# Kernel optimization log

Hardware: AMD Instinct MI355X
Metric: run time of the kernel (lower is better)

## Reference

```python
import jax, jax.numpy as jnp
import numpy as np

D_MODEL = 1024
NHEAD = 16
HEAD_DIM = D_MODEL // NHEAD
D_FF = 4096
BIAS_HID = 8
EPS = 1e-5


def _pair_bias(m, w1, b1, w2, b2):
    # m: [B,S,S] -> bias [B,S,S,nhead] via per-scalar MLP 1->hid->nhead
    h = jax.nn.relu(m[..., None] * w1 + b1)          # [B,S,S,hid]
    return jnp.einsum('bxyh,hn->bxyn', h, w2) + b2   # [B,S,S,nhead]


def _layernorm(x, g, b):
    mu = jnp.mean(x, axis=-1, keepdims=True)
    var = jnp.mean(jnp.square(x - mu), axis=-1, keepdims=True)
    return (x - mu) * jax.lax.rsqrt(var + EPS) * g + b


def setup_inputs() -> dict:
    key = jax.random.key(0)
    ks = jax.random.split(key, 20)
    B, S = 4, 1024
    sc = 1.0 / np.sqrt(D_MODEL)
    inp = {
        'src': jax.random.normal(ks[0], (B, S, D_MODEL), jnp.float32),
        't_deltas': jax.random.uniform(ks[1], (B, S, S), jnp.float32),
        'dists': jax.random.uniform(ks[2], (B, S, S), jnp.float32),
        'Wq': jax.random.normal(ks[3], (D_MODEL, D_MODEL), jnp.float32) * sc,
        'bq': jnp.zeros((D_MODEL,), jnp.float32),
        'Wk': jax.random.normal(ks[4], (D_MODEL, D_MODEL), jnp.float32) * sc,
        'bk': jnp.zeros((D_MODEL,), jnp.float32),
        'Wv': jax.random.normal(ks[5], (D_MODEL, D_MODEL), jnp.float32) * sc,
        'bv': jnp.zeros((D_MODEL,), jnp.float32),
        'tb_w1': jax.random.normal(ks[6], (BIAS_HID,), jnp.float32),
        'tb_b1': jnp.zeros((BIAS_HID,), jnp.float32),
        'tb_w2': jax.random.normal(ks[7], (BIAS_HID, NHEAD), jnp.float32) * 0.3,
        'tb_b2': jnp.zeros((NHEAD,), jnp.float32),
        'db_w1': jax.random.normal(ks[8], (BIAS_HID,), jnp.float32),
        'db_b1': jnp.zeros((BIAS_HID,), jnp.float32),
        'db_w2': jax.random.normal(ks[9], (BIAS_HID, NHEAD), jnp.float32) * 0.3,
        'db_b2': jnp.zeros((NHEAD,), jnp.float32),
        'W1': jax.random.normal(ks[10], (D_MODEL, D_FF), jnp.float32) * sc,
        'b1': jnp.zeros((D_FF,), jnp.float32),
        'W2': jax.random.normal(ks[11], (D_FF, D_MODEL), jnp.float32) / np.sqrt(D_FF),
        'b2': jnp.zeros((D_MODEL,), jnp.float32),
        'g1': jnp.ones((D_MODEL,), jnp.float32),
        'beta1': jnp.zeros((D_MODEL,), jnp.float32),
        'g2': jnp.ones((D_MODEL,), jnp.float32),
        'beta2': jnp.zeros((D_MODEL,), jnp.float32),
    }
    return inp


def reference(src, t_deltas, dists, Wq, bq, Wk, bk, Wv, bv,
              tb_w1, tb_b1, tb_w2, tb_b2, db_w1, db_b1, db_w2, db_b2,
              W1, b1, W2, b2, g1, beta1, g2, beta2):
    B, S, _ = src.shape
    # QKV projections -> [B, H, S, hd]
    q = (src @ Wq + bq).reshape(B, S, NHEAD, HEAD_DIM).transpose(0, 2, 1, 3)
    k = (src @ Wk + bk).reshape(B, S, NHEAD, HEAD_DIM).transpose(0, 2, 1, 3)
    v = (src @ Wv + bv).reshape(B, S, NHEAD, HEAD_DIM).transpose(0, 2, 1, 3)
    # scores scaled by sqrt(d_model) (as in the original, not head_dim)
    scores = jnp.einsum('bhqd,bhkd->bhqk', q, k) / jnp.sqrt(jnp.float32(D_MODEL))
    bias = (_pair_bias(t_deltas, tb_w1, tb_b1, tb_w2, tb_b2)
            + _pair_bias(dists, db_w1, db_b1, db_w2, db_b2))  # [B,S,S,H]
    scores = scores + bias.transpose(0, 3, 1, 2)
    attn = jax.nn.softmax(scores, axis=-1)
    out = jnp.einsum('bhqk,bhkd->bhqd', attn, v)
    out = out.transpose(0, 2, 1, 3).reshape(B, S, D_MODEL)
    x = _layernorm(src + out, g1, beta1)
    ffn = jax.nn.relu(x @ W1 + b1) @ W2 + b2
    return _layernorm(x + ffn, g2, beta2)
```

## Files before the change

kernel.cpp:

```cpp
#include <hip/hip_runtime.h>

typedef __bf16 bf16x8 __attribute__((ext_vector_type(8)));
typedef float f32x4 __attribute__((ext_vector_type(4)));
typedef unsigned short u16;

__device__ __forceinline__ u16 f2bf(float f) {
  union { float f; unsigned u; } x; x.f = f;
  unsigned r = x.u + 0x7fffu + ((x.u >> 16) & 1u);
  return (u16)(r >> 16);
}
__device__ __forceinline__ float bf2f(u16 u) {
  union { unsigned u; float f; } x; x.u = ((unsigned)u) << 16;
  return x.f;
}
__device__ __forceinline__ void gl_lds16(const void* g, void* l) {
  __builtin_amdgcn_global_load_lds(
      (const __attribute__((address_space(1))) void*)g,
      (__attribute__((address_space(3))) void*)l, 16, 0, 0);
}

__global__ __launch_bounds__(256) void cvt_kernel(const float* __restrict__ in,
                                                  u16* __restrict__ out, int n4) {
  int i = blockIdx.x * 256 + threadIdx.x;
  if (i >= n4) return;
  float4 v = ((const float4*)in)[i];
  unsigned lo = (unsigned)f2bf(v.x) | ((unsigned)f2bf(v.y) << 16);
  unsigned hi = (unsigned)f2bf(v.z) | ((unsigned)f2bf(v.w) << 16);
  uint2 u; u.x = lo; u.y = hi;
  *(uint2*)&out[(size_t)i * 4] = u;
}

__global__ __launch_bounds__(256) void tconv_kernel(const float* __restrict__ in,
                                                    u16* __restrict__ out, int R, int C) {
  __shared__ float tile[32][33];
  int c0 = blockIdx.x * 32, r0 = blockIdx.y * 32;
  int tx = threadIdx.x & 31, ty = threadIdx.x >> 5;
#pragma unroll
  for (int i = 0; i < 4; i++)
    tile[ty + i * 8][tx] = in[(size_t)(r0 + ty + i * 8) * C + c0 + tx];
  __syncthreads();
#pragma unroll
  for (int i = 0; i < 4; i++)
    out[(size_t)(c0 + ty + i * 8) * R + r0 + tx] = f2bf(tile[tx][ty + i * 8]);
}

__global__ __launch_bounds__(256) void tconv3_kernel(const float* __restrict__ w0,
                                                     const float* __restrict__ w1,
                                                     const float* __restrict__ w2,
                                                     u16* __restrict__ out) {
  __shared__ float tile[32][33];
  int mat = blockIdx.y >> 5;
  const float* in = mat == 0 ? w0 : (mat == 1 ? w1 : w2);
  u16* o = out + (size_t)mat * 1024 * 1024;
  int c0 = blockIdx.x * 32, r0 = (blockIdx.y & 31) * 32;
  int tx = threadIdx.x & 31, ty = threadIdx.x >> 5;
#pragma unroll
  for (int i = 0; i < 4; i++)
    tile[ty + i * 8][tx] = in[(size_t)(r0 + ty + i * 8) * 1024 + c0 + tx];
  __syncthreads();
#pragma unroll
  for (int i = 0; i < 4; i++)
    o[(size_t)(c0 + ty + i * 8) * 1024 + r0 + tx] = f2bf(tile[tx][ty + i * 8]);
}

template <int EPI>
__global__ __launch_bounds__(256) void gemm128_kernel(const u16* __restrict__ A,
                                                      const u16* __restrict__ Bt,
                                                      const float* __restrict__ bias,
                                                      const float* __restrict__ biasK,
                                                      const float* __restrict__ biasV,
                                                      void* __restrict__ out,
                                                      int M, int N, int K,
                                                      float qscale, int kslice) {
  __shared__ u16 lds[3][2][4096];
  int tid = threadIdx.x, w = tid >> 6, lane = tid & 63;
  int l16 = lane & 15, lhi = lane >> 4;
  int wr = w >> 1, wc = w & 1;
  int GX = gridDim.x;
  int nwg = GX * gridDim.y;
  int nlin = blockIdx.y * GX + blockIdx.x;
  int cpx = nwg >> 3;
  int sw = (nlin & 7) * cpx + (nlin >> 3);
  int m0 = (sw / GX) * 128, n0 = (sw % GX) * 128;
  int z = blockIdx.z;
  const u16* Ag = A + (size_t)m0 * K + z * kslice;
  const u16* Bg = Bt + (size_t)n0 * K + z * kslice;
  f32x4 acc[4][4] = {};
  int np = kslice >> 5;

  int srow = tid >> 2;
  int sxor = ((tid & 3) ^ ((tid >> 3) & 3)) * 8;
  int rga = (lhi ^ ((l16 >> 1) & 3)) * 8;

  auto stageP = [&](int slot, int p) {
    const u16* As = Ag + (size_t)p * 32 + sxor;
    const u16* Bs = Bg + (size_t)p * 32 + sxor;
#pragma unroll
    for (int ld = 0; ld < 2; ld++)
      gl_lds16(As + (size_t)(ld * 64 + srow) * K, &lds[slot][0][ld * 2048 + w * 512]);
#pragma unroll
    for (int ld = 0; ld < 2; ld++)
      gl_lds16(Bs + (size_t)(ld * 64 + srow) * K, &lds[slot][1][ld * 2048 + w * 512]);
  };
  auto rdAB = [&](int slot, bf16x8 (&af)[4], bf16x8 (&bfr)[4]) {
#pragma unroll
    for (int m = 0; m < 4; m++)
      af[m] = *(const bf16x8*)&lds[slot][0][(wr * 64 + m * 16 + l16) * 32 + rga];
#pragma unroll
    for (int nn = 0; nn < 4; nn++)
      bfr[nn] = *(const bf16x8*)&lds[slot][1][(wc * 64 + nn * 16 + l16) * 32 + rga];
  };
  auto mma16 = [&](bf16x8 (&af)[4], bf16x8 (&bfr)[4]) {
    __builtin_amdgcn_s_setprio(1);
#pragma unroll
    for (int m = 0; m < 4; m++)
#pragma unroll
      for (int nn = 0; nn < 4; nn++)
        acc[m][nn] =
            __builtin_amdgcn_mfma_f32_16x16x32_bf16(af[m], bfr[nn], acc[m][nn], 0, 0, 0);
    __builtin_amdgcn_s_setprio(0);
  };

  stageP(0, 0);
  stageP(1, 1);

  int slot = 0;
  for (int p = 0; p < np; ++p) {
    bf16x8 af[4], bfr[4];
    if (p + 1 < np) asm volatile("s_waitcnt vmcnt(4)" ::: "memory");
    else            asm volatile("s_waitcnt vmcnt(0)" ::: "memory");
    __builtin_amdgcn_s_barrier();
    rdAB(slot, af, bfr);
    if (p + 2 < np) {
      int s2 = slot + 2; if (s2 >= 3) s2 -= 3;
      stageP(s2, p + 2);
    }
    asm volatile("s_waitcnt lgkmcnt(0)" ::: "memory");
    __builtin_amdgcn_sched_barrier(0);
    mma16(af, bfr);
    if (++slot == 3) slot = 0;
  }

#pragma unroll
  for (int m = 0; m < 4; m++) {
    int gr = m0 + wr * 64 + m * 16 + lhi * 4;
#pragma unroll
    for (int nn = 0; nn < 4; nn++) {
      int gc = n0 + wc * 64 + nn * 16 + l16;
      float bv;
      if (EPI == 2) {
        int seg = gc >> 10, c = gc & 1023;
        bv = seg == 0 ? bias[c] : (seg == 1 ? biasK[c] : biasV[c]);
        int h = c >> 6, d = c & 63;
        float sc = (seg == 0) ? qscale : 1.f;
#pragma unroll
        for (int r = 0; r < 4; r++) {
          int row = gr + r;
          int b = row >> 10, s = row & 1023;
          size_t idx = ((((size_t)seg * 4 + b) * 16 + h) * 1024 + s) * 64 + d;
          ((u16*)out)[idx] = f2bf((acc[m][nn][r] + bv) * sc);
        }
      } else if (EPI == 1) {
        bv = bias[gc];
#pragma unroll
        for (int r = 0; r < 4; r++)
          ((u16*)out)[(size_t)(gr + r) * N + gc] = f2bf(fmaxf(acc[m][nn][r] + bv, 0.f));
      } else if (EPI == 3) {
        bv = (z == 0 && bias) ? bias[gc] : 0.f;
#pragma unroll
        for (int r = 0; r < 4; r++)
          ((u16*)out)[(size_t)z * M * N + (size_t)(gr + r) * N + gc] = f2bf(acc[m][nn][r] + bv);
      } else {
        bv = (z == 0 && bias) ? bias[gc] : 0.f;
#pragma unroll
        for (int r = 0; r < 4; r++)
          ((float*)out)[(size_t)z * M * N + (size_t)(gr + r) * N + gc] = acc[m][nn][r] + bv;
      }
    }
  }
}

__global__ __launch_bounds__(256) void vtrans_kernel(const u16* __restrict__ v,
                                                     u16* __restrict__ vt) {
  __shared__ u16 t[64][72];
  int bh = blockIdx.y, s0 = blockIdx.x * 64;
  int tid = threadIdx.x;
  int r = tid >> 2, c = (tid & 3) * 16;
  const u16* src = v + ((size_t)bh * 1024 + s0 + r) * 64 + c;
  *(int4*)&t[r][c] = *(const int4*)src;
  *(int4*)&t[r][c + 8] = *(const int4*)(src + 8);
  __syncthreads();
  int d = tid >> 2, sc = (tid & 3) * 16;
  u16 tmp[16];
#pragma unroll
  for (int j = 0; j < 16; j++) tmp[j] = t[sc + j][d];
  u16* dst = vt + ((size_t)bh * 64 + d) * 1024 + s0 + sc;
  *(int4*)dst = *(int4*)&tmp[0];
  *(int4*)(dst + 8) = *(int4*)&tmp[8];
}

#define LOG2E 1.44269504088896f
__global__ __launch_bounds__(256) void bias_kernel(
    const float* __restrict__ td, const float* __restrict__ dd,
    const float* __restrict__ tw1, const float* __restrict__ tb1,
    const float* __restrict__ tw2, const float* __restrict__ tb2,
    const float* __restrict__ dw1, const float* __restrict__ db1,
    const float* __restrict__ dw2, const float* __restrict__ db2,
    u16* __restrict__ biasout, int b0) {
  __shared__ float stw2[128], sdw2[128], sb2[16];
  __shared__ float stw1[8], stb1[8], sdw1[8], sdb1[8];
  int tid = threadIdx.x, x = blockIdx.x, bz = blockIdx.y;
  int b = b0 + bz;
  if (tid < 128) { stw2[tid] = tw2[tid]; sdw2[tid] = dw2[tid]; }
  if (tid < 16) sb2[tid] = tb2[tid] + db2[tid];
  if (tid < 8) { stw1[tid] = tw1[tid]; stb1[tid] = tb1[tid]; sdw1[tid] = dw1[tid]; sdb1[tid] = db1[tid]; }
  __syncthreads();
  float4 tv = ((const float4*)(td + ((size_t)b * 1024 + x) * 1024))[tid];
  float4 dv = ((const float4*)(dd + ((size_t)b * 1024 + x) * 1024))[tid];
  float tj[4] = {tv.x, tv.y, tv.z, tv.w};
  float dj[4] = {dv.x, dv.y, dv.z, dv.w};
  float ht[4][8], hd[4][8];
#pragma unroll
  for (int j = 0; j < 4; j++)
#pragma unroll
    for (int i = 0; i < 8; i++) {
      ht[j][i] = fmaxf(tj[j] * stw1[i] + stb1[i], 0.f);
      hd[j][i] = fmaxf(dj[j] * sdw1[i] + sdb1[i], 0.f);
    }
  u16* outb = biasout + (size_t)bz * 16 * 1024 * 1024 + (size_t)x * 1024 + tid * 4;
#pragma unroll
  for (int h = 0; h < 16; h++) {
    float a[4];
#pragma unroll
    for (int j = 0; j < 4; j++) {
      float s = sb2[h];
#pragma unroll
      for (int i = 0; i < 8; i++)
        s += ht[j][i] * stw2[i * 16 + h] + hd[j][i] * sdw2[i * 16 + h];
      a[j] = s * LOG2E;
    }
    unsigned lo = (unsigned)f2bf(a[0]) | ((unsigned)f2bf(a[1]) << 16);
    unsigned hi = (unsigned)f2bf(a[2]) | ((unsigned)f2bf(a[3]) << 16);
    uint2 u; u.x = lo; u.y = hi;
    *(uint2*)&outb[(size_t)h * 1024 * 1024] = u;
  }
}

#define LDA 72
#define SMC 12.0f
__global__ __launch_bounds__(256) void attn_kernel(
    const u16* __restrict__ qg, const u16* __restrict__ kg, const u16* __restrict__ vtg,
    const u16* __restrict__ bias, float* __restrict__ attn_out, int b0) {
  __shared__ u16 Ks[64 * LDA];
  __shared__ u16 Vt[64 * LDA];
  __shared__ u16 Ps[64 * LDA];
  int tid = threadIdx.x;
  int w = tid >> 6, l = tid & 63, l16 = l & 15, lhi = l >> 4;
  int qt = blockIdx.x, h = blockIdx.y, bz = blockIdx.z;
  int b = b0 + bz;
  size_t bh = ((size_t)(b * 16 + h)) * 1024 * 64;
  const u16* biasb = bias + (size_t)bz * 16 * 1024 * 1024 + (size_t)h * 1024 * 1024;
  int qrow = qt * 64 + w * 16 + l16;
  bf16x8 qa[2];
  qa[0] = *(const bf16x8*)&qg[bh + (size_t)qrow * 64 + lhi * 8];
  qa[1] = *(const bf16x8*)&qg[bh + (size_t)qrow * 64 + 32 + lhi * 8];

  float l_part[4] = {0.f, 0.f, 0.f, 0.f};
  f32x4 o[4] = {};

  int kr0 = (tid * 2) >> 3, kc0 = ((tid * 2) & 7) * 8;
  int kr1 = (tid * 2 + 1) >> 3, kc1 = ((tid * 2 + 1) & 7) * 8;
  const u16* kbase = kg + bh;
  const u16* vbase = vtg + bh;

  int4 kA, kB, vA, vB;
  u16 bpre[16];
  auto issueKV = [&](int kt) {
    kA = *(const int4*)&kbase[(size_t)(kt * 64 + kr0) * 64 + kc0];
    kB = *(const int4*)&kbase[(size_t)(kt * 64 + kr1) * 64 + kc1];
    vA = *(const int4*)&vbase[(size_t)kr0 * 1024 + kt * 64 + kc0];
    vB = *(const int4*)&vbase[(size_t)kr1 * 1024 + kt * 64 + kc1];
  };
  auto issueBias = [&](int kt) {
#pragma unroll
    for (int ni = 0; ni < 4; ni++)
#pragma unroll
      for (int r = 0; r < 4; r++)
        bpre[ni * 4 + r] =
            biasb[(size_t)(qt * 64 + w * 16 + lhi * 4 + r) * 1024 + kt * 64 + ni * 16 + l16];
  };
  issueKV(0);
  issueBias(0);

  for (int kt = 0; kt < 16; kt++) {
    __syncthreads();
    *(int4*)&Ks[kr0 * LDA + kc0] = kA;
    *(int4*)&Ks[kr1 * LDA + kc1] = kB;
    *(int4*)&Vt[kr0 * LDA + kc0] = vA;
    *(int4*)&Vt[kr1 * LDA + kc1] = vB;
    __syncthreads();
    u16 bcur[16];
#pragma unroll
    for (int i = 0; i < 16; i++) bcur[i] = bpre[i];
    if (kt + 1 < 16) { issueKV(kt + 1); issueBias(kt + 1); }
    __builtin_amdgcn_sched_barrier(0);

    f32x4 s[4] = {};
    __builtin_amdgcn_s_setprio(1);
#pragma unroll
    for (int ni = 0; ni < 4; ni++)
#pragma unroll
      for (int ks = 0; ks < 2; ks++) {
        bf16x8 kb = *(const bf16x8*)&Ks[(ni * 16 + l16) * LDA + ks * 32 + lhi * 8];
        s[ni] = __builtin_amdgcn_mfma_f32_16x16x32_bf16(qa[ks], kb, s[ni], 0, 0, 0);
      }
    __builtin_amdgcn_s_setprio(0);
#pragma unroll
    for (int ni = 0; ni < 4; ni++)
#pragma unroll
      for (int r = 0; r < 4; r++) {
        float p = exp2f(s[ni][r] + bf2f(bcur[ni * 4 + r]) - SMC);
        l_part[r] += p;
        Ps[(w * 16 + lhi * 4 + r) * LDA + ni * 16 + l16] = f2bf(p);
      }
    __builtin_amdgcn_s_setprio(1);
#pragma unroll
    for (int ks = 0; ks < 2; ks++) {
      bf16x8 pa = *(const bf16x8*)&Ps[(w * 16 + l16) * LDA + ks * 32 + lhi * 8];
#pragma unroll
      for (int di = 0; di < 4; di++) {
        bf16x8 vb = *(const bf16x8*)&Vt[(di * 16 + l16) * LDA + ks * 32 + lhi * 8];
        o[di] = __builtin_amdgcn_mfma_f32_16x16x32_bf16(pa, vb, o[di], 0, 0, 0);
      }
    }
    __builtin_amdgcn_s_setprio(0);
  }
#pragma unroll
  for (int r = 0; r < 4; r++) {
    float lr = l_part[r];
    lr += __shfl_xor(lr, 1, 16);
    lr += __shfl_xor(lr, 2, 16);
    lr += __shfl_xor(lr, 4, 16);
    lr += __shfl_xor(lr, 8, 16);
    float inv = 1.f / lr;
    int row = b * 1024 + qt * 64 + w * 16 + lhi * 4 + r;
#pragma unroll
    for (int di = 0; di < 4; di++)
      attn_out[(size_t)row * 1024 + h * 64 + di * 16 + l16] = o[di][r] * inv;
  }
}

__global__ __launch_bounds__(256) void ln_kernel(const float* __restrict__ a,
                                                 const float* __restrict__ r1,
                                                 const float* __restrict__ g,
                                                 const float* __restrict__ beta,
                                                 float* __restrict__ outf,
                                                 u16* __restrict__ outbf) {
  int row = blockIdx.x, tid = threadIdx.x;
  __shared__ float red[8];
  float4 va = ((const float4*)(a + (size_t)row * 1024))[tid];
  float4 vr = ((const float4*)(r1 + (size_t)row * 1024))[tid];
  float v[4] = {va.x + vr.x, va.y + vr.y, va.z + vr.z, va.w + vr.w};
  float s = v[0] + v[1] + v[2] + v[3];
#pragma unroll
  for (int off = 32; off >= 1; off >>= 1) s += __shfl_xor(s, off, 64);
  if ((tid & 63) == 0) red[tid >> 6] = s;
  __syncthreads();
  float mean = (red[0] + red[1] + red[2] + red[3]) * (1.f / 1024.f);
  float q = 0.f;
#pragma unroll
  for (int j = 0; j < 4; j++) { float d = v[j] - mean; q += d * d; }
#pragma unroll
  for (int off = 32; off >= 1; off >>= 1) q += __shfl_xor(q, off, 64);
  if ((tid & 63) == 0) red[4 + (tid >> 6)] = q;
  __syncthreads();
  float var = (red[4] + red[5] + red[6] + red[7]) * (1.f / 1024.f);
  float rstd = rsqrtf(var + 1e-5f);
  float4 gv = ((const float4*)g)[tid];
  float4 bv = ((const float4*)beta)[tid];
  float o0 = (v[0] - mean) * rstd * gv.x + bv.x;
  float o1 = (v[1] - mean) * rstd * gv.y + bv.y;
  float o2 = (v[2] - mean) * rstd * gv.z + bv.z;
  float o3 = (v[3] - mean) * rstd * gv.w + bv.w;
  float4 ov; ov.x = o0; ov.y = o1; ov.z = o2; ov.w = o3;
  ((float4*)(outf + (size_t)row * 1024))[tid] = ov;
  unsigned lo = (unsigned)f2bf(o0) | ((unsigned)f2bf(o1) << 16);
  unsigned hi = (unsigned)f2bf(o2) | ((unsigned)f2bf(o3) << 16);
  uint2 u; u.x = lo; u.y = hi;
  *(uint2*)&outbf[(size_t)row * 1024 + tid * 4] = u;
}

__global__ __launch_bounds__(256) void ln2_kernel(const float* __restrict__ x,
                                                  const u16* __restrict__ ff, int zs,
                                                  const float* __restrict__ g,
                                                  const float* __restrict__ beta,
                                                  float* __restrict__ out) {
  int row = blockIdx.x, tid = threadIdx.x;
  __shared__ float red[8];
  float4 xv = ((const float4*)(x + (size_t)row * 1024))[tid];
  float v[4] = {xv.x, xv.y, xv.z, xv.w};
  for (int z = 0; z < zs; z++) {
    uint2 u = *(const uint2*)&ff[(size_t)z * 4096 * 1024 + (size_t)row * 1024 + tid * 4];
    v[0] += bf2f(u.x & 0xffff); v[1] += bf2f(u.x >> 16);
    v[2] += bf2f(u.y & 0xffff); v[3] += bf2f(u.y >> 16);
  }
  float s = v[0] + v[1] + v[2] + v[3];
#pragma unroll
  for (int off = 32; off >= 1; off >>= 1) s += __shfl_xor(s, off, 64);
  if ((tid & 63) == 0) red[tid >> 6] = s;
  __syncthreads();
  float mean = (red[0] + red[1] + red[2] + red[3]) * (1.f / 1024.f);
  float q = 0.f;
#pragma unroll
  for (int j = 0; j < 4; j++) { float d = v[j] - mean; q += d * d; }
#pragma unroll
  for (int off = 32; off >= 1; off >>= 1) q += __shfl_xor(q, off, 64);
  if ((tid & 63) == 0) red[4 + (tid >> 6)] = q;
  __syncthreads();
  float var = (red[4] + red[5] + red[6] + red[7]) * (1.f / 1024.f);
  float rstd = rsqrtf(var + 1e-5f);
  float4 gv = ((const float4*)g)[tid];
  float4 bv = ((const float4*)beta)[tid];
  float4 ov;
  ov.x = (v[0] - mean) * rstd * gv.x + bv.x;
  ov.y = (v[1] - mean) * rstd * gv.y + bv.y;
  ov.z = (v[2] - mean) * rstd * gv.z + bv.z;
  ov.w = (v[3] - mean) * rstd * gv.w + bv.w;
  ((float4*)(out + (size_t)row * 1024))[tid] = ov;
}

extern "C" void kernel_launch(void* const* d_in, const int* in_sizes, int n_in,
                              void* d_out, int out_size, void* d_ws, size_t ws_size,
                              hipStream_t stream) {
  const float* src      = (const float*)d_in[0];
  const float* t_deltas = (const float*)d_in[1];
  const float* dists    = (const float*)d_in[2];
  const float* Wq = (const float*)d_in[3];
  const float* bq = (const float*)d_in[4];
  const float* Wk = (const float*)d_in[5];
  const float* bk = (const float*)d_in[6];
  const float* Wv = (const float*)d_in[7];
  const float* bv = (const float*)d_in[8];
  const float* tb_w1 = (const float*)d_in[9];
  const float* tb_b1 = (const float*)d_in[10];
  const float* tb_w2 = (const float*)d_in[11];
  const float* tb_b2 = (const float*)d_in[12];
  const float* db_w1 = (const float*)d_in[13];
  const float* db_b1 = (const float*)d_in[14];
  const float* db_w2 = (const float*)d_in[15];
  const float* db_b2 = (const float*)d_in[16];
  const float* W1 = (const float*)d_in[17];
  const float* b1 = (const float*)d_in[18];
  const float* W2 = (const float*)d_in[19];
  const float* b2 = (const float*)d_in[20];
  const float* g1 = (const float*)d_in[21];
  const float* beta1 = (const float*)d_in[22];
  const float* g2 = (const float*)d_in[23];
  const float* beta2 = (const float*)d_in[24];
  float* out = (float*)d_out;

  const size_t MB = 1024u * 1024;
  bool huge = ws_size >= 210 * MB;
  bool big  = ws_size >= 150 * MB;
  int PB = huge ? 4 : (big ? 2 : 1);
  const int ZS = 2;

  char* ws = (char*)d_ws;
  size_t off = 0;
  auto alloc = [&](size_t n) { void* p = ws + off; off += (n + 255) & ~(size_t)255; return p; };
  u16* src_bf  = (u16*)alloc(4096u * 1024 * 2);
  u16* wqkv_bt = (u16*)alloc(3072u * 1024 * 2);
  u16* w1_bt   = (u16*)alloc(4096u * 1024 * 2);
  u16* w2_bt   = (u16*)alloc(1024u * 4096 * 2);
  u16* qkv     = (u16*)alloc(3u * 4 * 16 * 1024 * 64 * 2);
  u16* vt      = (u16*)alloc(4u * 16 * 64 * 1024 * 2);
  u16* slab    = (u16*)alloc((size_t)PB * 16 * 1024 * 1024 * 2);
  float* attn_out = (float*)alloc(4096u * 1024 * 4);
  (void)in_sizes; (void)n_in; (void)out_size;

  u16* q_bf = qkv;
  u16* k_bf = qkv + 4u * 16 * 1024 * 64;
  u16* v_bf = qkv + 8u * 16 * 1024 * 64;
  float* x_f32 = (float*)qkv;
  u16*   x_bf  = (u16*)((char*)qkv + 16 * MB);
  u16*   h_bf  = (u16*)vt;
  u16*   ffnb  = (u16*)attn_out;

  cvt_kernel<<<4096, 256, 0, stream>>>(src, src_bf, 4096 * 1024 / 4);
  tconv3_kernel<<<dim3(32, 96), 256, 0, stream>>>(Wq, Wk, Wv, wqkv_bt);
  tconv_kernel<<<dim3(128, 32), 256, 0, stream>>>(W1, w1_bt, 1024, 4096);
  tconv_kernel<<<dim3(32, 128), 256, 0, stream>>>(W2, w2_bt, 4096, 1024);

  gemm128_kernel<2><<<dim3(24, 32, 1), 256, 0, stream>>>(src_bf, wqkv_bt, bq, bk, bv, qkv,
                                                         4096, 3072, 1024,
                                                         1.44269504088896f / 32.f, 1024);
  vtrans_kernel<<<dim3(16, 64), 256, 0, stream>>>(v_bf, vt);

  for (int p = 0; p < 4 / PB; p++) {
    bias_kernel<<<dim3(1024, PB), 256, 0, stream>>>(t_deltas, dists, tb_w1, tb_b1, tb_w2, tb_b2,
                                                    db_w1, db_b1, db_w2, db_b2, slab, p * PB);
    attn_kernel<<<dim3(16, 16, PB), 256, 0, stream>>>(q_bf, k_bf, vt, slab, attn_out, p * PB);
  }

  ln_kernel<<<4096, 256, 0, stream>>>(src, attn_out, g1, beta1, x_f32, x_bf);
  gemm128_kernel<1><<<dim3(32, 32, 1), 256, 0, stream>>>(x_bf, w1_bt, b1, nullptr, nullptr, h_bf,
                                                         4096, 4096, 1024, 1.f, 1024);
  gemm128_kernel<3><<<dim3(8, 32, ZS), 256, 0, stream>>>(h_bf, w2_bt, b2, nullptr, nullptr, ffnb,
                                                         4096, 1024, 4096, 1.f, 4096 / ZS);
  ln2_kernel<<<4096, 256, 0, stream>>>(x_f32, ffnb, ZS, g2, beta2, out);
}
```

Baseline: 281.2 us.

## Store pair bias in MFMA fragment order for vectorized attention loads

The bias kernel now writes the bf16 bias slab in the per-thread fragment order used by the attention kernel's MFMA accumulator layout. Each attention thread can then fetch its 16 bias values with two 16-byte loads instead of 16 scattered 2-byte loads. The trade-off is that the bias kernel now reads t_deltas and dists with strided scalar loads instead of coalesced float4 row loads, and the grid is reshaped to 16x16 tiles. The bias index inside the softmax loop is permuted to match the new packing.

After: 612.1 us. 2.18x slower.

```diff
diff --git a/kernel.cpp b/kernel.cpp
--- a/kernel.cpp
+++ b/kernel.cpp
@@ -209,40 +209,49 @@
     u16* __restrict__ biasout, int b0) {
   __shared__ float stw2[128], sdw2[128], sb2[16];
   __shared__ float stw1[8], stb1[8], sdw1[8], sdb1[8];
-  int tid = threadIdx.x, x = blockIdx.x, bz = blockIdx.y;
+  int tid = threadIdx.x;
+  int kt = blockIdx.x, qt = blockIdx.y, bz = blockIdx.z;
   int b = b0 + bz;
   if (tid < 128) { stw2[tid] = tw2[tid]; sdw2[tid] = dw2[tid]; }
   if (tid < 16) sb2[tid] = tb2[tid] + db2[tid];
   if (tid < 8) { stw1[tid] = tw1[tid]; stb1[tid] = tb1[tid]; sdw1[tid] = dw1[tid]; sdb1[tid] = db1[tid]; }
   __syncthreads();
-  float4 tv = ((const float4*)(td + ((size_t)b * 1024 + x) * 1024))[tid];
-  float4 dv = ((const float4*)(dd + ((size_t)b * 1024 + x) * 1024))[tid];
-  float tj[4] = {tv.x, tv.y, tv.z, tv.w};
-  float dj[4] = {dv.x, dv.y, dv.z, dv.w};
-  float ht[4][8], hd[4][8];
-#pragma unroll
-  for (int j = 0; j < 4; j++)
-#pragma unroll
-    for (int i = 0; i < 8; i++) {
-      ht[j][i] = fmaxf(tj[j] * stw1[i] + stb1[i], 0.f);
-      hd[j][i] = fmaxf(dj[j] * sdw1[i] + sdb1[i], 0.f);
+  int w = tid >> 6, l = tid & 63, lhi = l >> 4, l16 = l & 15;
+  u16* outb = biasout + ((((size_t)bz * 16 * 16 + qt) * 16 + kt) * 256 + tid) * 16;
+  const size_t hstride = (size_t)16 * 16 * 256 * 16;
+
+#pragma unroll
+  for (int r = 0; r < 4; r++) {
+    int x = qt * 64 + w * 16 + lhi * 4 + r;
+    const float* trow = td + ((size_t)b * 1024 + x) * 1024 + kt * 64 + l16;
+    const float* drow = dd + ((size_t)b * 1024 + x) * 1024 + kt * 64 + l16;
+    float tj[4], dj[4];
+#pragma unroll
+    for (int ni = 0; ni < 4; ni++) { tj[ni] = trow[ni * 16]; dj[ni] = drow[ni * 16]; }
+    float ht[4][8], hd[4][8];
+#pragma unroll
+    for (int ni = 0; ni < 4; ni++)
+#pragma unroll
+      for (int i = 0; i < 8; i++) {
+        ht[ni][i] = fmaxf(tj[ni] * stw1[i] + stb1[i], 0.f);
+        hd[ni][i] = fmaxf(dj[ni] * sdw1[i] + sdb1[i], 0.f);
+      }
+#pragma unroll
+    for (int h = 0; h < 16; h++) {
+      float a[4];
+#pragma unroll
+      for (int ni = 0; ni < 4; ni++) {
+        float s = sb2[h];
+#pragma unroll
+        for (int i = 0; i < 8; i++)
+          s += ht[ni][i] * stw2[i * 16 + h] + hd[ni][i] * sdw2[i * 16 + h];
+        a[ni] = s * LOG2E;
+      }
+      uint2 u;
+      u.x = (unsigned)f2bf(a[0]) | ((unsigned)f2bf(a[1]) << 16);
+      u.y = (unsigned)f2bf(a[2]) | ((unsigned)f2bf(a[3]) << 16);
+      *(uint2*)&outb[hstride * h + r * 4] = u;
     }
-  u16* outb = biasout + (size_t)bz * 16 * 1024 * 1024 + (size_t)x * 1024 + tid * 4;
-#pragma unroll
-  for (int h = 0; h < 16; h++) {
-    float a[4];
-#pragma unroll
-    for (int j = 0; j < 4; j++) {
-      float s = sb2[h];
-#pragma unroll
-      for (int i = 0; i < 8; i++)
-        s += ht[j][i] * stw2[i * 16 + h] + hd[j][i] * sdw2[i * 16 + h];
-      a[j] = s * LOG2E;
-    }
-    unsigned lo = (unsigned)f2bf(a[0]) | ((unsigned)f2bf(a[1]) << 16);
-    unsigned hi = (unsigned)f2bf(a[2]) | ((unsigned)f2bf(a[3]) << 16);
-    uint2 u; u.x = lo; u.y = hi;
-    *(uint2*)&outb[(size_t)h * 1024 * 1024] = u;
   }
 }
 
@@ -259,7 +268,7 @@
   int qt = blockIdx.x, h = blockIdx.y, bz = blockIdx.z;
   int b = b0 + bz;
   size_t bh = ((size_t)(b * 16 + h)) * 1024 * 64;
-  const u16* biasb = bias + (size_t)bz * 16 * 1024 * 1024 + (size_t)h * 1024 * 1024;
+  const u16* bfragbase = bias + ((((size_t)(bz * 16 + h) * 16 + qt) * 16) * 256 + tid) * 16;
   int qrow = qt * 64 + w * 16 + l16;
   bf16x8 qa[2];
   qa[0] = *(const bf16x8*)&qg[bh + (size_t)qrow * 64 + lhi * 8];
@@ -274,7 +283,7 @@
   const u16* vbase = vtg + bh;
 
   int4 kA, kB, vA, vB;
-  u16 bpre[16];
+  int4 bp0, bp1;
   auto issueKV = [&](int kt) {
     kA = *(const int4*)&kbase[(size_t)(kt * 64 + kr0) * 64 + kc0];
     kB = *(const int4*)&kbase[(size_t)(kt * 64 + kr1) * 64 + kc1];
@@ -282,12 +291,9 @@
     vB = *(const int4*)&vbase[(size_t)kr1 * 1024 + kt * 64 + kc1];
   };
   auto issueBias = [&](int kt) {
-#pragma unroll
-    for (int ni = 0; ni < 4; ni++)
-#pragma unroll
-      for (int r = 0; r < 4; r++)
-        bpre[ni * 4 + r] =
-            biasb[(size_t)(qt * 64 + w * 16 + lhi * 4 + r) * 1024 + kt * 64 + ni * 16 + l16];
+    const int4* p = (const int4*)(bfragbase + (size_t)kt * 256 * 16);
+    bp0 = p[0];
+    bp1 = p[1];
   };
   issueKV(0);
   issueBias(0);
@@ -300,8 +306,8 @@
     *(int4*)&Vt[kr1 * LDA + kc1] = vB;
     __syncthreads();
     u16 bcur[16];
-#pragma unroll
-    for (int i = 0; i < 16; i++) bcur[i] = bpre[i];
+    *(int4*)&bcur[0] = bp0;
+    *(int4*)&bcur[8] = bp1;
     if (kt + 1 < 16) { issueKV(kt + 1); issueBias(kt + 1); }
     __builtin_amdgcn_sched_barrier(0);
 
@@ -319,7 +325,7 @@
     for (int ni = 0; ni < 4; ni++)
 #pragma unroll
       for (int r = 0; r < 4; r++) {
-        float p = exp2f(s[ni][r] + bf2f(bcur[ni * 4 + r]) - SMC);
+        float p = exp2f(s[ni][r] + bf2f(bcur[r * 4 + ni]) - SMC);
         l_part[r] += p;
         Ps[(w * 16 + lhi * 4 + r) * LDA + ni * 16 + l16] = f2bf(p);
       }
@@ -497,8 +503,8 @@
   vtrans_kernel<<<dim3(16, 64), 256, 0, stream>>>(v_bf, vt);
 
   for (int p = 0; p < 4 / PB; p++) {
-    bias_kernel<<<dim3(1024, PB), 256, 0, stream>>>(t_deltas, dists, tb_w1, tb_b1, tb_w2, tb_b2,
-                                                    db_w1, db_b1, db_w2, db_b2, slab, p * PB);
+    bias_kernel<<<dim3(16, 16, PB), 256, 0, stream>>>(t_deltas, dists, tb_w1, tb_b1, tb_w2, tb_b2,
+                                                      db_w1, db_b1, db_w2, db_b2, slab, p * PB);
     attn_kernel<<<dim3(16, 16, PB), 256, 0, stream>>>(q_bf, k_bf, vt, slab, attn_out, p * PB);
   }
 
```
